# Kernel tuning notes

Hardware: AMD Instinct MI355X
Metric: run time of the kernel (lower is better)

Reference implementation:

```python
import jax, jax.numpy as jnp
import numpy as np
from jax import lax

TAU_MEM = 100.0   # 1/0.01 default
V_LEAK = 0.0
V_TH = 1.0


def setup_inputs() -> dict:
    key = jax.random.key(0)
    k1, k2 = jax.random.split(key)
    B, T, F = 32, 128, 2048
    inp = jax.random.normal(k1, (B, T, F), dtype=jnp.float32)
    W = jax.random.normal(k2, (F, F), dtype=jnp.float32) * (1.0 / np.sqrt(F))
    b = jnp.zeros((F,), dtype=jnp.float32)
    return {"input": inp, "W": W, "b": b}


def _heaviside(x):
    return (x > 0).astype(x.dtype)


def reference(input, W, b):
    # time-distributed kernel: Linear applied to all timesteps at once
    gs = jnp.einsum('btn,mn->btm', input, W) + b  # [B, T, F]
    dt_over_tau = 1.0 / TAU_MEM

    def step(v, g):
        # Euler LIF update with delta (subtractive) reset
        v_new = v + dt_over_tau * ((V_LEAK - v) + g)
        z = _heaviside(v_new - V_TH)
        v_reset = v_new - z * V_TH
        return v_reset, z

    v0 = jnp.zeros(gs.shape[::2], dtype=gs.dtype)  # [B, F]
    _, zs = lax.scan(step, v0, jnp.moveaxis(gs, 1, 0))  # zs: [T, B, F]
    return jnp.moveaxis(zs, 0, 1)  # [B, T, F]
```

## Files before the change

### kernel.cpp

```cpp
#include <hip/hip_runtime.h>
#include <hip/hip_bf16.h>
#include <stdint.h>

#define Bdim 32
#define Tdim 128
#define Fdim 2048
#define Mdim (Bdim*Tdim)

#define BM 128
#define BN 128
#define BK 64

typedef __attribute__((ext_vector_type(8))) short bf16x8;
typedef __attribute__((ext_vector_type(4))) float f32x4;

__device__ inline unsigned short f2bf(float f) {
    union { float f; unsigned u; } x; x.f = f;
    unsigned r = (x.u + 0x7fffu + ((x.u >> 16) & 1u)) >> 16;
    return (unsigned short)r;
}

__global__ void convert_kernel(const float* __restrict__ A, const float* __restrict__ W,
                               unsigned short* __restrict__ a16, unsigned short* __restrict__ w16) {
    const int nA4 = (Mdim * Fdim) / 4;
    const int nW4 = (Fdim * Fdim) / 4;
    const int stride = gridDim.x * blockDim.x;
    for (int i = blockIdx.x * blockDim.x + threadIdx.x; i < nA4 + nW4; i += stride) {
        const float4* src; unsigned short* dst; int j;
        if (i < nA4) { src = (const float4*)A; dst = a16; j = i; }
        else         { src = (const float4*)W; dst = w16; j = i - nA4; }
        float4 v = src[j];
        ushort4 o;
        o.x = f2bf(v.x); o.y = f2bf(v.y); o.z = f2bf(v.z); o.w = f2bf(v.w);
        *(ushort4*)(dst + 4 * (size_t)j) = o;
    }
}

__global__ __launch_bounds__(256) void gemm_fused_kernel(const unsigned short* __restrict__ A,
                                                         const unsigned short* __restrict__ Wm,
                                                         const float* __restrict__ bias,
                                                         float* __restrict__ Z) {
    __shared__ __align__(16) char smem[128 * 132 * 4];

    const int tid = threadIdx.x;
    const int wid = tid >> 6, lane = tid & 63;
    const int wr = wid >> 1, wc = wid & 1;
    const int m0 = blockIdx.y * BM, n0 = blockIdx.x * BN;

    f32x4 acc[4][4];
#pragma unroll
    for (int i = 0; i < 4; i++)
#pragma unroll
        for (int j = 0; j < 4; j++) acc[i][j] = f32x4{0.f, 0.f, 0.f, 0.f};

    const int frow = lane & 15;
    const int lgrp = lane >> 4;

    auto stage = [&](int buf, int kt) {
        const int k0 = kt * BK;
        char* sAb = smem + buf * 16384;
        char* sBb = smem + 32768 + buf * 16384;
#pragma unroll
        for (int j = 0; j < 4; ++j) {
            const int base = wid * 1024 + j * 4096;
            const int off  = base + lane * 16;
            const int row  = off >> 7;
            const int chk  = (off & 127) >> 4;
            const int scol = ((chk ^ (row & 7)) << 3);
            const unsigned short* ga = A  + (size_t)(m0 + row) * Fdim + k0 + scol;
            const unsigned short* gb = Wm + (size_t)(n0 + row) * Fdim + k0 + scol;
            __builtin_amdgcn_global_load_lds(
                (const __attribute__((address_space(1))) void*)ga,
                (__attribute__((address_space(3))) void*)(sAb + base), 16, 0, 0);
            __builtin_amdgcn_global_load_lds(
                (const __attribute__((address_space(1))) void*)gb,
                (__attribute__((address_space(3))) void*)(sBb + base), 16, 0, 0);
        }
    };

    stage(0, 0);
    __syncthreads();

    int cur = 0;
    const int NT = Fdim / BK;
    for (int kt = 0; kt < NT; ++kt) {
        if (kt + 1 < NT) stage(cur ^ 1, kt + 1);

        const unsigned short* sAc = (const unsigned short*)(smem + cur * 16384);
        const unsigned short* sBc = (const unsigned short*)(smem + 32768 + cur * 16384);
        bf16x8 af[2][4], bfr[2][4];
#pragma unroll
        for (int kk = 0; kk < 2; kk++) {
            const int chunk = kk * 4 + lgrp;
#pragma unroll
            for (int mi = 0; mi < 4; mi++) {
                const int r = wr * 64 + mi * 16 + frow;
                af[kk][mi] = *(const bf16x8*)(sAc + r * BK + ((chunk ^ (r & 7)) << 3));
            }
#pragma unroll
            for (int ni = 0; ni < 4; ni++) {
                const int r = wc * 64 + ni * 16 + frow;
                bfr[kk][ni] = *(const bf16x8*)(sBc + r * BK + ((chunk ^ (r & 7)) << 3));
            }
        }
#pragma unroll
        for (int kk = 0; kk < 2; kk++)
#pragma unroll
            for (int mi = 0; mi < 4; mi++)
#pragma unroll
                for (int ni = 0; ni < 4; ni++)
                    acc[mi][ni] = __builtin_amdgcn_mfma_f32_16x16x32_bf16(af[kk][mi], bfr[kk][ni], acc[mi][ni], 0, 0, 0);

        __syncthreads();
        cur ^= 1;
    }

    float* ct = (float*)smem;
#pragma unroll
    for (int mi = 0; mi < 4; mi++)
#pragma unroll
        for (int ni = 0; ni < 4; ni++) {
            const int r0 = wr * 64 + mi * 16 + (lane >> 4) * 4;
            const int c0 = wc * 64 + ni * 16 + (lane & 15);
#pragma unroll
            for (int r = 0; r < 4; r++) ct[(r0 + r) * 132 + c0] = acc[mi][ni][r];
        }
    __syncthreads();

    if (tid < 128) {
        const int gcol = n0 + tid;
        const float bf = bias[gcol];
        float* outp = Z + (size_t)m0 * Fdim + gcol;
        float v = 0.f;
#pragma unroll 16
        for (int t = 0; t < Tdim; t++) {
            const float g = ct[t * 132 + tid] + bf;
            const float vn = v + 0.01f * ((0.0f - v) + g);
            const float z = (vn > 1.0f) ? 1.0f : 0.0f;
            v = vn - z;
            outp[(size_t)t * Fdim] = z;
        }
    }
}

__global__ void gemm_f32_naive(const float* __restrict__ A, const float* __restrict__ W,
                               float* __restrict__ C) {
    int col = blockIdx.x * blockDim.x + threadIdx.x;
    int row = blockIdx.y;
    float s = 0.f;
    for (int k = 0; k < Fdim; k++) s += A[(size_t)row * Fdim + k] * W[(size_t)col * Fdim + k];
    C[(size_t)row * Fdim + col] = s;
}

__global__ __launch_bounds__(256, 1) void lif_kernel(float* __restrict__ gs,
                                                     const float* __restrict__ bias) {
    int idx = blockIdx.x * blockDim.x + threadIdx.x;
    int b = idx >> 11, f = idx & (Fdim - 1);
    const float bf = bias[f];
    float* p = gs + (size_t)b * Tdim * Fdim + f;
    float v = 0.f;
#pragma unroll 16
    for (int t = 0; t < Tdim; t++) {
        float g = p[(size_t)t * Fdim] + bf;
        float vn = v + 0.01f * ((0.0f - v) + g);
        float z = (vn > 1.0f) ? 1.0f : 0.0f;
        v = vn - z;
        p[(size_t)t * Fdim] = z;
    }
}

extern "C" void kernel_launch(void* const* d_in, const int* in_sizes, int n_in,
                              void* d_out, int out_size, void* d_ws, size_t ws_size,
                              hipStream_t stream) {
    const float* inp  = (const float*)d_in[0];
    const float* W    = (const float*)d_in[1];
    const float* bias = (const float*)d_in[2];
    float* out = (float*)d_out;

    const size_t needA = (size_t)Mdim * Fdim * 2;
    const size_t needW = (size_t)Fdim * Fdim * 2;

    if (ws_size >= needA + needW) {
        unsigned short* a16 = (unsigned short*)d_ws;
        unsigned short* w16 = (unsigned short*)((char*)d_ws + needA);
        convert_kernel<<<2048, 256, 0, stream>>>(inp, W, a16, w16);
        dim3 grid(Fdim / BN, Mdim / BM);
        gemm_fused_kernel<<<grid, 256, 0, stream>>>(a16, w16, bias, out);
    } else {
        dim3 grid(Fdim / 256, Mdim);
        gemm_f32_naive<<<grid, 256, 0, stream>>>(inp, W, out);
        lif_kernel<<<(Bdim * Fdim) / 256, 256, 0, stream>>>(out, bias);
    }
}
```

Baseline: 139.8 us.

## Enlarge GEMM tile to 256x128 with 8 waves and triple-buffered LDS pipeline

Doubles the M tile to 256 rows and launches 512 threads (8 waves) per block. The K loop now runs a three-stage LDS buffer rotation: prefetches are issued two tiles ahead, partial `s_waitcnt vmcnt` waits replace full drains, and a single barrier per iteration replaces two `__syncthreads`. The aim is to hide global-to-LDS latency better and raise data reuse per block. The cost is about 144KB of LDS per block, which allows only one block per CU. The grid also shrinks to 256 blocks, so one block per CU may leave little room for tail balancing. The LIF epilogue is split across two 128-row halves.

```diff
diff --git a/kernel.cpp b/kernel.cpp
--- a/kernel.cpp
+++ b/kernel.cpp
@@ -7,9 +7,10 @@
 #define Fdim 2048
 #define Mdim (Bdim*Tdim)
 
-#define BM 128
+#define BM 256
 #define BN 128
 #define BK 64
+#define NT (Fdim/BK)
 
 typedef __attribute__((ext_vector_type(8))) short bf16x8;
 typedef __attribute__((ext_vector_type(4))) float f32x4;
@@ -36,11 +37,11 @@
     }
 }
 
-__global__ __launch_bounds__(256) void gemm_fused_kernel(const unsigned short* __restrict__ A,
-                                                         const unsigned short* __restrict__ Wm,
-                                                         const float* __restrict__ bias,
-                                                         float* __restrict__ Z) {
-    __shared__ __align__(16) char smem[128 * 132 * 4];
+__global__ __launch_bounds__(512, 2) void gemm_fused_kernel(const unsigned short* __restrict__ A,
+                                                            const unsigned short* __restrict__ Wm,
+                                                            const float* __restrict__ bias,
+                                                            float* __restrict__ Z) {
+    __shared__ __align__(16) char smem[147456];
 
     const int tid = threadIdx.x;
     const int wid = tid >> 6, lane = tid & 63;
@@ -58,20 +59,28 @@
 
     auto stage = [&](int buf, int kt) {
         const int k0 = kt * BK;
-        char* sAb = smem + buf * 16384;
-        char* sBb = smem + 32768 + buf * 16384;
+        char* sAb = smem + buf * 49152;
+        char* sBb = sAb + 32768;
 #pragma unroll
         for (int j = 0; j < 4; ++j) {
-            const int base = wid * 1024 + j * 4096;
+            const int base = wid * 4096 + j * 1024;
             const int off  = base + lane * 16;
             const int row  = off >> 7;
             const int chk  = (off & 127) >> 4;
-            const int scol = ((chk ^ (row & 7)) << 3);
-            const unsigned short* ga = A  + (size_t)(m0 + row) * Fdim + k0 + scol;
-            const unsigned short* gb = Wm + (size_t)(n0 + row) * Fdim + k0 + scol;
+            const int scol = (chk ^ (row & 7)) << 3;
+            const unsigned short* ga = A + (size_t)(m0 + row) * Fdim + k0 + scol;
             __builtin_amdgcn_global_load_lds(
                 (const __attribute__((address_space(1))) void*)ga,
                 (__attribute__((address_space(3))) void*)(sAb + base), 16, 0, 0);
+        }
+#pragma unroll
+        for (int j = 0; j < 2; ++j) {
+            const int base = wid * 2048 + j * 1024;
+            const int off  = base + lane * 16;
+            const int row  = off >> 7;
+            const int chk  = (off & 127) >> 4;
+            const int scol = (chk ^ (row & 7)) << 3;
+            const unsigned short* gb = Wm + (size_t)(n0 + row) * Fdim + k0 + scol;
             __builtin_amdgcn_global_load_lds(
                 (const __attribute__((address_space(1))) void*)gb,
                 (__attribute__((address_space(3))) void*)(sBb + base), 16, 0, 0);
@@ -79,15 +88,18 @@
     };
 
     stage(0, 0);
-    __syncthreads();
-
-    int cur = 0;
-    const int NT = Fdim / BK;
-    for (int kt = 0; kt < NT; ++kt) {
-        if (kt + 1 < NT) stage(cur ^ 1, kt + 1);
-
-        const unsigned short* sAc = (const unsigned short*)(smem + cur * 16384);
-        const unsigned short* sBc = (const unsigned short*)(smem + 32768 + cur * 16384);
+    stage(1, 1);
+
+#pragma unroll 1
+    for (int t = 0; t < NT; ++t) {
+        if (t < NT - 1) asm volatile("s_waitcnt vmcnt(6)" ::: "memory");
+        else            asm volatile("s_waitcnt vmcnt(0)" ::: "memory");
+        __builtin_amdgcn_s_barrier();
+        __builtin_amdgcn_sched_barrier(0);
+        if (t + 2 < NT) stage((t + 2) % 3, t + 2);
+
+        const unsigned short* sAc = (const unsigned short*)(smem + (t % 3) * 49152);
+        const unsigned short* sBc = (const unsigned short*)(smem + (t % 3) * 49152 + 32768);
         bf16x8 af[2][4], bfr[2][4];
 #pragma unroll
         for (int kk = 0; kk < 2; kk++) {
@@ -110,10 +122,9 @@
 #pragma unroll
                 for (int ni = 0; ni < 4; ni++)
                     acc[mi][ni] = __builtin_amdgcn_mfma_f32_16x16x32_bf16(af[kk][mi], bfr[kk][ni], acc[mi][ni], 0, 0, 0);
-
-        __syncthreads();
-        cur ^= 1;
-    }
+    }
+
+    __syncthreads();
 
     float* ct = (float*)smem;
 #pragma unroll
@@ -127,14 +138,16 @@
         }
     __syncthreads();
 
-    if (tid < 128) {
-        const int gcol = n0 + tid;
+    if (tid < 256) {
+        const int sub  = tid >> 7;
+        const int col  = tid & 127;
+        const int gcol = n0 + col;
         const float bf = bias[gcol];
-        float* outp = Z + (size_t)m0 * Fdim + gcol;
+        float* outp = Z + (size_t)(m0 + sub * 128) * Fdim + gcol;
         float v = 0.f;
 #pragma unroll 16
         for (int t = 0; t < Tdim; t++) {
-            const float g = ct[t * 132 + tid] + bf;
+            const float g = ct[(sub * 128 + t) * 132 + col] + bf;
             const float vn = v + 0.01f * ((0.0f - v) + g);
             const float z = (vn > 1.0f) ? 1.0f : 0.0f;
             v = vn - z;
@@ -185,7 +198,7 @@
         unsigned short* w16 = (unsigned short*)((char*)d_ws + needA);
         convert_kernel<<<2048, 256, 0, stream>>>(inp, W, a16, w16);
         dim3 grid(Fdim / BN, Mdim / BM);
-        gemm_fused_kernel<<<grid, 256, 0, stream>>>(a16, w16, bias, out);
+        gemm_fused_kernel<<<grid, 512, 0, stream>>>(a16, w16, bias, out);
     } else {
         dim3 grid(Fdim / 256, Mdim);
         gemm_f32_naive<<<grid, 256, 0, stream>>>(inp, W, out);
```

New measurement: 134.3 us. 3.9% less time.
